# Performance work log

Hardware: AMD Instinct MI355X
Metric: run time of the kernel (lower is better)

Reference implementation:

```python
import jax, jax.numpy as jnp
import numpy as np

B, N, D, H, NCTX = 4, 2048, 1024, 16, 512
HD = D // H  # head dim = 64


def setup_inputs() -> dict:
    key = jax.random.key(0)
    ks = jax.random.split(key, 6)
    return {
        "x": jax.random.normal(ks[0], (B, N, D), dtype=jnp.float32),
        "ctx_ppr": jax.random.uniform(ks[1], (B, NCTX), dtype=jnp.float32),
        "ctx_trust": jax.random.normal(ks[2], (B, NCTX), dtype=jnp.float32),
        "W_in": jax.random.normal(ks[3], (D, 3 * D), dtype=jnp.float32) * 0.02,
        "b_in": jnp.zeros((3 * D,), dtype=jnp.float32),
        "W_out": jax.random.normal(ks[4], (D, D), dtype=jnp.float32) * 0.02,
        "b_out": jnp.zeros((D,), dtype=jnp.float32),
        "log_ppr_alpha": jnp.full((1,), 0.1, dtype=jnp.float32),
        "trust_scale": jnp.full((1,), 0.1, dtype=jnp.float32),
        "n_ctx": NCTX,
    }


def reference(x, ctx_ppr, ctx_trust, W_in, b_in, W_out, b_out, log_ppr_alpha, trust_scale, n_ctx):
    b, n, dmodel = x.shape
    # QKV projection
    qkv = x @ W_in + b_in                                   # [B,N,3D]
    q, k, v = jnp.split(qkv, 3, axis=-1)
    q = q.reshape(b, n, H, HD).transpose(0, 2, 1, 3)        # [B,H,N,d]
    k = k.reshape(b, n, H, HD).transpose(0, 2, 1, 3)
    v = v.reshape(b, n, H, HD).transpose(0, 2, 1, 3)
    if n_ctx > 0:
        # multiplicative trust gate on context-token values
        gate = jax.nn.sigmoid(trust_scale * ctx_trust)      # [B,n_ctx]
        gate_full = jnp.concatenate(
            [gate, jnp.ones((b, n - n_ctx), dtype=x.dtype)], axis=1)  # [B,N]
        v = v * gate_full[:, None, :, None]
        # additive graph (log-PPR) column bias on attention logits
        col_bias = -log_ppr_alpha * jnp.log(jnp.maximum(ctx_ppr, 1e-8))  # [B,n_ctx]
        bias = jnp.concatenate(
            [col_bias, jnp.zeros((b, n - n_ctx), dtype=x.dtype)], axis=1)  # [B,N]
    else:
        bias = jnp.zeros((b, n), dtype=x.dtype)
    scale = 1.0 / np.sqrt(HD).astype(np.float32)
    scores = jnp.einsum("bhqd,bhkd->bhqk", q, k) * scale + bias[:, None, None, :]
    attn = jax.nn.softmax(scores, axis=-1)                  # [B,H,N,N]
    out = jnp.einsum("bhqk,bhkd->bhqd", attn, v)            # [B,H,N,d]
    out = out.transpose(0, 2, 1, 3).reshape(b, n, dmodel)
    return out @ W_out + b_out
```

## Files before the change

kernel.cpp:

```cpp
#include <hip/hip_runtime.h>
#include <hip/hip_bf16.h>
#include <stdint.h>

#define BATCH  4
#define NSEQ   2048
#define DMODEL 1024
#define NHEAD  16
#define HDIM   64
#define NCTXC  512

typedef unsigned short u16;
typedef __attribute__((ext_vector_type(8))) short bfrag;
typedef __attribute__((ext_vector_type(4))) float facc;

typedef __attribute__((address_space(3))) void lds_void;
typedef __attribute__((address_space(1))) void g_void;

__device__ __forceinline__ void gload16(const void* g, void* l) {
  __builtin_amdgcn_global_load_lds((const g_void*)g, (lds_void*)l, 16, 0, 0);
}

__device__ __forceinline__ u16 f2bf(float f) {
  union { float f; uint32_t u; } un; un.f = f;
  uint32_t u = un.u;
  u += 0x7fffu + ((u >> 16) & 1u);
  return (u16)(u >> 16);
}

#if __has_builtin(__builtin_amdgcn_cvt_pk_bf16_f32)
__device__ __forceinline__ uint32_t pk2bf(float a, float b) {
  return __builtin_bit_cast(uint32_t, __builtin_amdgcn_cvt_pk_bf16_f32(a, b));
}
#else
__device__ __forceinline__ uint32_t pk2bf(float a, float b) {
  return (uint32_t)f2bf(a) | ((uint32_t)f2bf(b) << 16);
}
#endif

__device__ __forceinline__ float bf2f(u16 h) {
  union { uint32_t u; float f; } un;
  un.u = ((uint32_t)h) << 16;
  return un.f;
}

__device__ __forceinline__ float load_flex(const void* p, size_t idx, int isb) {
  return isb ? bf2f(((const u16*)p)[idx]) : ((const float*)p)[idx];
}

__device__ __forceinline__ uint4 pack8(float4 a, float4 b) {
  uint4 r;
  r.x = pk2bf(a.x, a.y);
  r.y = pk2bf(a.z, a.w);
  r.z = pk2bf(b.x, b.y);
  r.w = pk2bf(b.z, b.w);
  return r;
}

__global__ __launch_bounds__(256) void detect_kernel(const u16* __restrict__ xraw,
                                                     int* __restrict__ flag) {
  __shared__ int s_high, s_zero;
  if (threadIdx.x == 0) { s_high = 0; s_zero = 0; }
  __syncthreads();
  int h = 0, z = 0;
  for (int i = threadIdx.x; i < 4096; i += 256) {
    const u16 v = xraw[2 * i];
    const int e = (v >> 7) & 0xFF;
    if (e >= 0x90) h++;
    if (v == 0) z++;
  }
  atomicAdd(&s_high, h);
  atomicAdd(&s_zero, z);
  __syncthreads();
  if (threadIdx.x == 0) flag[0] = (s_high < 64 && s_zero < 2048) ? 1 : 0;
}


__global__ __launch_bounds__(256) void cast_x_kernel(const void* __restrict__ x,
                                                     u16* __restrict__ xb,
                                                     const int* __restrict__ flag) {
  const int isb = flag[0];
  const int i = blockIdx.x * 256 + threadIdx.x;
  if (isb) {
    ((uint4*)xb)[i] = ((const uint4*)x)[i];
  } else {
    const float4 f0 = ((const float4*)x)[2 * i];
    const float4 f1 = ((const float4*)x)[2 * i + 1];
    ((uint4*)xb)[i] = pack8(f0, f1);
  }
}

__global__ __launch_bounds__(256) void transpose_flex(const void* __restrict__ W,
                                                      u16* __restrict__ Wt,
                                                      int R, int C,
                                                      const int* __restrict__ flag) {
  __shared__ float tile[32][33];
  const int isb = flag[0];
  const int tx = threadIdx.x;
  const int ty = threadIdx.y;
  const int c0 = blockIdx.x * 32;
  const int r0 = blockIdx.y * 32;
#pragma unroll
  for (int j = 0; j < 32; j += 8)
    tile[ty + j][tx] = load_flex(W, (size_t)(r0 + ty + j) * C + c0 + tx, isb);
  __syncthreads();
#pragma unroll
  for (int j = 0; j < 32; j += 8)
    Wt[(size_t)(c0 + ty + j) * R + r0 + tx] = f2bf(tile[tx][ty + j]);
}

__global__ __launch_bounds__(256) void prep_small(const void* __restrict__ b_in,
                                                  const void* __restrict__ b_out,
                                                  const void* __restrict__ ppr,
                                                  const void* __restrict__ trust,
                                                  const void* __restrict__ alpha_p,
                                                  const void* __restrict__ ts_p,
                                                  float* __restrict__ bin_f,
                                                  float* __restrict__ bout_f,
                                                  float* __restrict__ gate,
                                                  float* __restrict__ cbias,
                                                  const int* __restrict__ flag) {
  const int isb = flag[0];
  const int i = blockIdx.x * 256 + threadIdx.x;
  if (i < 3072) {
    bin_f[i] = load_flex(b_in, i, isb);
  } else if (i < 4096) {
    bout_f[i - 3072] = load_flex(b_out, i - 3072, isb);
  } else if (i < 4096 + BATCH * NCTXC) {
    const int j = i - 4096;
    const float ts = load_flex(ts_p, 0, isb), al = load_flex(alpha_p, 0, isb);
    gate[j]  = 1.0f / (1.0f + __expf(-ts * load_flex(trust, j, isb)));
    cbias[j] = -al * logf(fmaxf(load_flex(ppr, j, isb), 1e-8f)) * 1.44269504f;
  }
}

__device__ __forceinline__ void kloop_mfma(const u16* __restrict__ Ag,
                                           const u16* __restrict__ Bg,
                                           u16* As, u16* Bs,
                                           int tid, int wM, int wN, int l16, int quad,
                                           facc acc[4][4]) {
  char* ldsA = (char*)As + tid * 16;
  char* ldsB = (char*)Bs + tid * 16;
  for (int k0 = 0; k0 < 1024; k0 += 32) {
    __syncthreads();
    gload16(Ag + k0, ldsA);
    gload16(Ag + (size_t)64 * 1024 + k0, ldsA + 4096);
    gload16(Bg + k0, ldsB);
    gload16(Bg + (size_t)64 * 1024 + k0, ldsB + 4096);
    __syncthreads();

    bfrag af[4], bf[4];
#pragma unroll
    for (int i = 0; i < 4; ++i)
      af[i] = *(const bfrag*)(&As[(wM + i * 16 + l16) * 32 + quad * 8]);
#pragma unroll
    for (int j = 0; j < 4; ++j)
      bf[j] = *(const bfrag*)(&Bs[(wN + j * 16 + l16) * 32 + quad * 8]);
#pragma unroll
    for (int i = 0; i < 4; ++i)
#pragma unroll
      for (int j = 0; j < 4; ++j)
        acc[i][j] = __builtin_amdgcn_mfma_f32_16x16x32_bf16(af[i], bf[j], acc[i][j], 0, 0, 0);
  }
}

__global__ __launch_bounds__(256) void gemm_qkvt(const u16* __restrict__ xb,
                                                 const u16* __restrict__ Wt,
                                                 const float* __restrict__ bin_f,
                                                 const float* __restrict__ gate,
                                                 u16* __restrict__ qk,
                                                 u16* __restrict__ Vtg) {
  __shared__ u16 As[128 * 32];
  __shared__ u16 Bs[128 * 32];
  const int tid  = threadIdx.x;
  const int w    = tid >> 6;
  const int lane = tid & 63;
  const int quad = lane >> 4;
  const int l16  = lane & 15;
  const int wM   = (w >> 1) * 64;
  const int wN   = (w & 1) * 64;
  const int id   = blockIdx.x;
  const int srow  = tid >> 2;
  const int spart = tid & 3;

  facc acc[4][4] = {};

  if (id < 1024) {
    const int bn = id & 15, bm = id >> 4;
    const u16* Ag = xb + (size_t)(bm * 128 + srow) * 1024 + spart * 8;
    const u16* Bg = Wt + (size_t)(bn * 128 + srow) * 1024 + spart * 8;
    kloop_mfma(Ag, Bg, As, Bs, tid, wM, wN, l16, quad, acc);

    const float qs = (bn < 8) ? 0.18033688f : 1.0f;
#pragma unroll
    for (int i = 0; i < 4; ++i) {
      const int grow0 = bm * 128 + wM + i * 16 + quad * 4;
#pragma unroll
      for (int j = 0; j < 4; ++j) {
        const int gcol = bn * 128 + wN + j * 16 + l16;
        const float bv = bin_f[gcol];
#pragma unroll
        for (int r = 0; r < 4; ++r)
          qk[(size_t)(grow0 + r) * 2048 + gcol] = f2bf((acc[i][j][r] + bv) * qs);
      }
    }
  } else {
    const int id2 = id - 1024;
    const int bn = id2 & 63, bm = id2 >> 6;
    const u16* Ag = Wt + (size_t)2048 * 1024 + (size_t)(bm * 128 + srow) * 1024 + spart * 8;
    const u16* Bg = xb + (size_t)(bn * 128 + srow) * 1024 + spart * 8;
    kloop_mfma(Ag, Bg, As, Bs, tid, wM, wN, l16, quad, acc);

#pragma unroll
    for (int i = 0; i < 4; ++i) {
      const int grow0 = bm * 128 + wM + i * 16 + quad * 4;
      const int h   = grow0 >> 6;
      const int dd0 = grow0 & 63;
#pragma unroll
      for (int j = 0; j < 4; ++j) {
        const int gcol = bn * 128 + wN + j * 16 + l16;
        const int bb  = gcol >> 11;
        const int tok = gcol & (NSEQ - 1);
        const float gl = (tok < NCTXC) ? gate[bb * NCTXC + tok] : 1.0f;
        u16* dst = &Vtg[((size_t)((bb * NHEAD + h) * HDIM + dd0)) * NSEQ + tok];
#pragma unroll
        for (int r = 0; r < 4; ++r)
          dst[(size_t)r * NSEQ] = f2bf((acc[i][j][r] + bin_f[2 * DMODEL + grow0 + r]) * gl);
      }
    }
  }
}

__global__ __launch_bounds__(256) void gemm_out(const u16* __restrict__ A,
                                                const u16* __restrict__ Bt,
                                                const float* __restrict__ biasf,
                                                void* __restrict__ Cout,
                                                const int* __restrict__ flag) {
  __shared__ u16 As[128 * 32];
  __shared__ u16 Bs[128 * 32];
  const int isb  = flag[0];
  const int tid  = threadIdx.x;
  const int w    = tid >> 6;
  const int lane = tid & 63;
  const int quad = lane >> 4;
  const int l16  = lane & 15;
  const int wM   = (w >> 1) * 64;
  const int wN   = (w & 1) * 64;
  const int bm   = blockIdx.y;
  const int bn   = blockIdx.x;
  const int srow  = tid >> 2;
  const int spart = tid & 3;

  facc acc[4][4] = {};
  const u16* Ag = A + (size_t)(bm * 128 + srow) * 2048 + spart * 8;
  const u16* Bg = Bt + (size_t)(bn * 128 + srow) * 1024 + spart * 8;
  char* ldsA = (char*)As + tid * 16;
  char* ldsB = (char*)Bs + tid * 16;

  for (int k0 = 0; k0 < 1024; k0 += 32) {
    __syncthreads();
    gload16(Ag + k0, ldsA);
    gload16(Ag + (size_t)64 * 2048 + k0, ldsA + 4096);
    gload16(Bg + k0, ldsB);
    gload16(Bg + (size_t)64 * 1024 + k0, ldsB + 4096);
    __syncthreads();

    bfrag af[4], bf[4];
#pragma unroll
    for (int i = 0; i < 4; ++i)
      af[i] = *(const bfrag*)(&As[(wM + i * 16 + l16) * 32 + quad * 8]);
#pragma unroll
    for (int j = 0; j < 4; ++j)
      bf[j] = *(const bfrag*)(&Bs[(wN + j * 16 + l16) * 32 + quad * 8]);
#pragma unroll
    for (int i = 0; i < 4; ++i)
#pragma unroll
      for (int j = 0; j < 4; ++j)
        acc[i][j] = __builtin_amdgcn_mfma_f32_16x16x32_bf16(af[i], bf[j], acc[i][j], 0, 0, 0);
  }

#pragma unroll
  for (int i = 0; i < 4; ++i) {
    const int grow0 = bm * 128 + wM + i * 16 + quad * 4;
#pragma unroll
    for (int j = 0; j < 4; ++j) {
      const int gcol = bn * 128 + wN + j * 16 + l16;
      const float bv = biasf[gcol];
#pragma unroll
      for (int r = 0; r < 4; ++r) {
        const float v = acc[i][j][r] + bv;
        if (isb) ((u16*)Cout)[(size_t)(grow0 + r) * 1024 + gcol] = f2bf(v);
        else     ((float*)Cout)[(size_t)(grow0 + r) * 1024 + gcol] = v;
      }
    }
  }
}

__global__ __launch_bounds__(256) void attn_kernel(u16* __restrict__ qk,
                                                   const u16* __restrict__ vtg,
                                                   const float* __restrict__ cbias) {
  const int qt = blockIdx.x, h = blockIdx.y, b = blockIdx.z;
  __shared__ u16 Ks[64 * 72];
  __shared__ u16 Vt[2][64 * 72];
  __shared__ u16 Ps[4 * 16 * 72];

  const int tid  = threadIdx.x;
  const int w    = tid >> 6;
  const int lane = tid & 63;
  const int quad = lane >> 4;
  const int l16  = lane & 15;
  const int srow = tid >> 2;
  const int spart = tid & 3;

  const u16* qrow = qk + (size_t)(b * NSEQ + qt * 64 + w * 16 + l16) * 2048 + h * HDIM;
  const bfrag bq0 = *(const bfrag*)(qrow + quad * 8);
  const bfrag bq1 = *(const bfrag*)(qrow + 32 + quad * 8);

  float l_i = 0.0f;
  facc o[4] = {};
  bfrag bp0, bp1;

  const u16* kst = qk + (size_t)(b * NSEQ) * 2048 + DMODEL + h * HDIM;
  const u16* vst = vtg + (size_t)((b * NHEAD + h) * HDIM + srow) * NSEQ;
  u16* psw = &Ps[w * 16 * 72];

  uint4 pk0, pk1, pv0, pv1;
  {
    const u16* ks = kst + (size_t)srow * 2048 + spart * 16;
    pk0 = *(const uint4*)ks;
    pk1 = *(const uint4*)(ks + 8);
    const u16* vs = vst + spart * 16;
    pv0 = *(const uint4*)vs;
    pv1 = *(const uint4*)(vs + 8);
  }

  for (int t = 0; t < NSEQ / 64; ++t) {
    __syncthreads();
    u16* vb = Vt[t & 1];
    *(uint4*)(&Ks[srow * 72 + spart * 16])     = pk0;
    *(uint4*)(&Ks[srow * 72 + spart * 16 + 8]) = pk1;
    *(uint4*)(&vb[srow * 72 + spart * 16])     = pv0;
    *(uint4*)(&vb[srow * 72 + spart * 16 + 8]) = pv1;
    __syncthreads();

    {
      const int tn = (t < NSEQ / 64 - 1) ? t + 1 : t;
      const u16* ks = kst + (size_t)(tn * 64 + srow) * 2048 + spart * 16;
      pk0 = *(const uint4*)ks;
      pk1 = *(const uint4*)(ks + 8);
      const u16* vs = vst + tn * 64 + spart * 16;
      pv0 = *(const uint4*)vs;
      pv1 = *(const uint4*)(vs + 8);
    }

    facc s[4];
#pragma unroll
    for (int nt = 0; nt < 4; ++nt) {
      const bfrag ak0 = *(const bfrag*)(&Ks[(nt * 16 + l16) * 72 + quad * 8]);
      const bfrag ak1 = *(const bfrag*)(&Ks[(nt * 16 + l16) * 72 + 32 + quad * 8]);
      facc z = {};
      z = __builtin_amdgcn_mfma_f32_16x16x32_bf16(ak0, bq0, z, 0, 0, 0);
      s[nt] = __builtin_amdgcn_mfma_f32_16x16x32_bf16(ak1, bq1, z, 0, 0, 0);
    }

    if (t > 0) {
      const u16* vp = Vt[(t - 1) & 1];
#pragma unroll
      for (int dt = 0; dt < 4; ++dt) {
        const bfrag av0 = *(const bfrag*)(&vp[(dt * 16 + l16) * 72 + quad * 8]);
        const bfrag av1 = *(const bfrag*)(&vp[(dt * 16 + l16) * 72 + 32 + quad * 8]);
        o[dt] = __builtin_amdgcn_mfma_f32_16x16x32_bf16(av0, bp0, o[dt], 0, 0, 0);
        o[dt] = __builtin_amdgcn_mfma_f32_16x16x32_bf16(av1, bp1, o[dt], 0, 0, 0);
      }
    }

    float rs = 0.0f;
    if (t < 8) {
      const float* cb = cbias + b * NCTXC + t * 64 + quad * 4;
#pragma unroll
      for (int nt = 0; nt < 4; ++nt)
#pragma unroll
        for (int r = 0; r < 4; ++r) {
          const float p = __builtin_amdgcn_exp2f(s[nt][r] + cb[nt * 16 + r]);
          s[nt][r] = p;
          rs += p;
        }
    } else {
#pragma unroll
      for (int nt = 0; nt < 4; ++nt)
#pragma unroll
        for (int r = 0; r < 4; ++r) {
          const float p = __builtin_amdgcn_exp2f(s[nt][r]);
          s[nt][r] = p;
          rs += p;
        }
    }
    rs += __shfl_xor(rs, 16);
    rs += __shfl_xor(rs, 32);
    l_i += rs;

#pragma unroll
    for (int nt = 0; nt < 4; ++nt) {
      uint2 pk;
      pk.x = pk2bf(s[nt][0], s[nt][1]);
      pk.y = pk2bf(s[nt][2], s[nt][3]);
      *(uint2*)(&psw[l16 * 72 + nt * 16 + quad * 4]) = pk;
    }
    __asm__ volatile("s_waitcnt lgkmcnt(0)" ::: "memory");
    bp0 = *(const bfrag*)(&psw[l16 * 72 + quad * 8]);
    bp1 = *(const bfrag*)(&psw[l16 * 72 + 32 + quad * 8]);
  }

  {
    const u16* vp = Vt[(NSEQ / 64 - 1) & 1];
#pragma unroll
    for (int dt = 0; dt < 4; ++dt) {
      const bfrag av0 = *(const bfrag*)(&vp[(dt * 16 + l16) * 72 + quad * 8]);
      const bfrag av1 = *(const bfrag*)(&vp[(dt * 16 + l16) * 72 + 32 + quad * 8]);
      o[dt] = __builtin_amdgcn_mfma_f32_16x16x32_bf16(av0, bp0, o[dt], 0, 0, 0);
      o[dt] = __builtin_amdgcn_mfma_f32_16x16x32_bf16(av1, bp1, o[dt], 0, 0, 0);
    }
  }

  const float inv = 1.0f / l_i;
  u16* orow = qk + (size_t)(b * NSEQ + qt * 64 + w * 16 + l16) * 2048 + h * HDIM;
#pragma unroll
  for (int dt = 0; dt < 4; ++dt) {
    uint2 st;
    st.x = pk2bf(o[dt][0] * inv, o[dt][1] * inv);
    st.y = pk2bf(o[dt][2] * inv, o[dt][3] * inv);
    *(uint2*)(orow + dt * 16 + quad * 4) = st;
  }
}


extern "C" void kernel_launch(void* const* d_in, const int* in_sizes, int n_in,
                              void* d_out, int out_size, void* d_ws, size_t ws_size,
                              hipStream_t stream) {
  const void* x          = d_in[0];
  const void* ctx_ppr    = d_in[1];
  const void* ctx_trust  = d_in[2];
  const void* W_in       = d_in[3];
  const void* b_in       = d_in[4];
  const void* W_out      = d_in[5];
  const void* b_out      = d_in[6];
  const void* lppr_alpha = d_in[7];
  const void* tscale     = d_in[8];

  char* ws = (char*)d_ws;
  u16* Wt    = (u16*)ws;  ws += (size_t)3072 * 1024 * 2;
  u16* WoT   = (u16*)ws;  ws += (size_t)1024 * 1024 * 2;
  u16* qk    = (u16*)ws;  ws += (size_t)8192 * 2048 * 2;
  u16* Vtg   = (u16*)ws;  ws += (size_t)64 * 64 * 2048 * 2;
  u16* xb    = (u16*)ws;  ws += (size_t)8192 * 1024 * 2;
  float* bin_f  = (float*)ws; ws += 3072 * 4;
  float* bout_f = (float*)ws; ws += 1024 * 4;
  float* gate   = (float*)ws; ws += (size_t)BATCH * NCTXC * 4;
  float* cbias  = (float*)ws; ws += (size_t)BATCH * NCTXC * 4;
  int*   flag   = (int*)ws;   ws += 64;

  detect_kernel<<<dim3(1), dim3(256), 0, stream>>>((const u16*)x, flag);
  cast_x_kernel<<<dim3(4096), dim3(256), 0, stream>>>(x, xb, flag);
  transpose_flex<<<dim3(96, 32), dim3(32, 8), 0, stream>>>(W_in, Wt, 1024, 3072, flag);
  transpose_flex<<<dim3(32, 32), dim3(32, 8), 0, stream>>>(W_out, WoT, 1024, 1024, flag);
  prep_small<<<dim3(24), dim3(256), 0, stream>>>(b_in, b_out, ctx_ppr, ctx_trust,
                                                 lppr_alpha, tscale,
                                                 bin_f, bout_f, gate, cbias, flag);
  gemm_qkvt<<<dim3(1536), dim3(256), 0, stream>>>(xb, Wt, bin_f, gate, qk, Vtg);
  attn_kernel<<<dim3(32, 16, 4), dim3(256), 0, stream>>>(qk, Vtg, cbias);
  gemm_out<<<dim3(8, 64), dim3(256), 0, stream>>>(qk, WoT, bout_f, d_out, flag);
}
```

Measured before the change: 338.4 us.

## Process 128 queries per attention block and swizzle block-to-head mapping

Measured after the change: 334.1 us. About the same (-1.2%).

```diff
diff --git a/kernel.cpp b/kernel.cpp
--- a/kernel.cpp
+++ b/kernel.cpp
@@ -298,9 +298,15 @@
 __global__ __launch_bounds__(256) void attn_kernel(u16* __restrict__ qk,
                                                    const u16* __restrict__ vtg,
                                                    const float* __restrict__ cbias) {
-  const int qt = blockIdx.x, h = blockIdx.y, b = blockIdx.z;
+  const int id    = blockIdx.x;
+  const int chunk = id >> 3;
+  const int qt    = chunk & 15;
+  const int hg    = (id & 7) | ((chunk >> 4) << 3);
+  const int h     = hg & 15;
+  const int b     = hg >> 4;
+
   __shared__ u16 Ks[64 * 72];
-  __shared__ u16 Vt[2][64 * 72];
+  __shared__ u16 Vt[64 * 72];
   __shared__ u16 Ps[4 * 16 * 72];
 
   const int tid  = threadIdx.x;
@@ -311,13 +317,16 @@
   const int srow = tid >> 2;
   const int spart = tid & 3;
 
-  const u16* qrow = qk + (size_t)(b * NSEQ + qt * 64 + w * 16 + l16) * 2048 + h * HDIM;
-  const bfrag bq0 = *(const bfrag*)(qrow + quad * 8);
-  const bfrag bq1 = *(const bfrag*)(qrow + 32 + quad * 8);
-
-  float l_i = 0.0f;
-  facc o[4] = {};
-  bfrag bp0, bp1;
+  bfrag bq[2][2];
+#pragma unroll
+  for (int qs = 0; qs < 2; ++qs) {
+    const u16* qrow = qk + (size_t)(b * NSEQ + qt * 128 + (w * 2 + qs) * 16 + l16) * 2048 + h * HDIM;
+    bq[qs][0] = *(const bfrag*)(qrow + quad * 8);
+    bq[qs][1] = *(const bfrag*)(qrow + 32 + quad * 8);
+  }
+
+  float l_i[2] = {0.0f, 0.0f};
+  facc o[2][4] = {};
 
   const u16* kst = qk + (size_t)(b * NSEQ) * 2048 + DMODEL + h * HDIM;
   const u16* vst = vtg + (size_t)((b * NHEAD + h) * HDIM + srow) * NSEQ;
@@ -335,11 +344,10 @@
 
   for (int t = 0; t < NSEQ / 64; ++t) {
     __syncthreads();
-    u16* vb = Vt[t & 1];
     *(uint4*)(&Ks[srow * 72 + spart * 16])     = pk0;
     *(uint4*)(&Ks[srow * 72 + spart * 16 + 8]) = pk1;
-    *(uint4*)(&vb[srow * 72 + spart * 16])     = pv0;
-    *(uint4*)(&vb[srow * 72 + spart * 16 + 8]) = pv1;
+    *(uint4*)(&Vt[srow * 72 + spart * 16])     = pv0;
+    *(uint4*)(&Vt[srow * 72 + spart * 16 + 8]) = pv1;
     __syncthreads();
 
     {
@@ -352,83 +360,81 @@
       pv1 = *(const uint4*)(vs + 8);
     }
 
-    facc s[4];
+    bfrag ak[4][2], av[4][2];
 #pragma unroll
     for (int nt = 0; nt < 4; ++nt) {
-      const bfrag ak0 = *(const bfrag*)(&Ks[(nt * 16 + l16) * 72 + quad * 8]);
-      const bfrag ak1 = *(const bfrag*)(&Ks[(nt * 16 + l16) * 72 + 32 + quad * 8]);
-      facc z = {};
-      z = __builtin_amdgcn_mfma_f32_16x16x32_bf16(ak0, bq0, z, 0, 0, 0);
-      s[nt] = __builtin_amdgcn_mfma_f32_16x16x32_bf16(ak1, bq1, z, 0, 0, 0);
-    }
-
-    if (t > 0) {
-      const u16* vp = Vt[(t - 1) & 1];
+      ak[nt][0] = *(const bfrag*)(&Ks[(nt * 16 + l16) * 72 + quad * 8]);
+      ak[nt][1] = *(const bfrag*)(&Ks[(nt * 16 + l16) * 72 + 32 + quad * 8]);
+      av[nt][0] = *(const bfrag*)(&Vt[(nt * 16 + l16) * 72 + quad * 8]);
+      av[nt][1] = *(const bfrag*)(&Vt[(nt * 16 + l16) * 72 + 32 + quad * 8]);
+    }
+
+#pragma unroll
+    for (int qs = 0; qs < 2; ++qs) {
+      facc s[4];
+#pragma unroll
+      for (int nt = 0; nt < 4; ++nt) {
+        facc z = {};
+        z = __builtin_amdgcn_mfma_f32_16x16x32_bf16(ak[nt][0], bq[qs][0], z, 0, 0, 0);
+        s[nt] = __builtin_amdgcn_mfma_f32_16x16x32_bf16(ak[nt][1], bq[qs][1], z, 0, 0, 0);
+      }
+
+      float rs = 0.0f;
+      if (t < 8) {
+        const float* cb = cbias + b * NCTXC + t * 64 + quad * 4;
+#pragma unroll
+        for (int nt = 0; nt < 4; ++nt)
+#pragma unroll
+          for (int r = 0; r < 4; ++r) {
+            const float p = __builtin_amdgcn_exp2f(s[nt][r] + cb[nt * 16 + r]);
+            s[nt][r] = p;
+            rs += p;
+          }
+      } else {
+#pragma unroll
+        for (int nt = 0; nt < 4; ++nt)
+#pragma unroll
+          for (int r = 0; r < 4; ++r) {
+            const float p = __builtin_amdgcn_exp2f(s[nt][r]);
+            s[nt][r] = p;
+            rs += p;
+          }
+      }
+      rs += __shfl_xor(rs, 16);
+      rs += __shfl_xor(rs, 32);
+      l_i[qs] += rs;
+
+#pragma unroll
+      for (int nt = 0; nt < 4; ++nt) {
+        uint2 pk;
+        pk.x = pk2bf(s[nt][0], s[nt][1]);
+        pk.y = pk2bf(s[nt][2], s[nt][3]);
+        *(uint2*)(&psw[l16 * 72 + nt * 16 + quad * 4]) = pk;
+      }
+
+      __asm__ volatile("s_waitcnt lgkmcnt(0)" ::: "memory");
+
+      const bfrag bp0 = *(const bfrag*)(&psw[l16 * 72 + quad * 8]);
+      const bfrag bp1 = *(const bfrag*)(&psw[l16 * 72 + 32 + quad * 8]);
 #pragma unroll
       for (int dt = 0; dt < 4; ++dt) {
-        const bfrag av0 = *(const bfrag*)(&vp[(dt * 16 + l16) * 72 + quad * 8]);
-        const bfrag av1 = *(const bfrag*)(&vp[(dt * 16 + l16) * 72 + 32 + quad * 8]);
-        o[dt] = __builtin_amdgcn_mfma_f32_16x16x32_bf16(av0, bp0, o[dt], 0, 0, 0);
-        o[dt] = __builtin_amdgcn_mfma_f32_16x16x32_bf16(av1, bp1, o[dt], 0, 0, 0);
-      }
-    }
-
-    float rs = 0.0f;
-    if (t < 8) {
-      const float* cb = cbias + b * NCTXC + t * 64 + quad * 4;
-#pragma unroll
-      for (int nt = 0; nt < 4; ++nt)
-#pragma unroll
-        for (int r = 0; r < 4; ++r) {
-          const float p = __builtin_amdgcn_exp2f(s[nt][r] + cb[nt * 16 + r]);
-          s[nt][r] = p;
-          rs += p;
-        }
-    } else {
-#pragma unroll
-      for (int nt = 0; nt < 4; ++nt)
-#pragma unroll
-        for (int r = 0; r < 4; ++r) {
-          const float p = __builtin_amdgcn_exp2f(s[nt][r]);
-          s[nt][r] = p;
-          rs += p;
-        }
-    }
-    rs += __shfl_xor(rs, 16);
-    rs += __shfl_xor(rs, 32);
-    l_i += rs;
-
-#pragma unroll
-    for (int nt = 0; nt < 4; ++nt) {
-      uint2 pk;
-      pk.x = pk2bf(s[nt][0], s[nt][1]);
-      pk.y = pk2bf(s[nt][2], s[nt][3]);
-      *(uint2*)(&psw[l16 * 72 + nt * 16 + quad * 4]) = pk;
-    }
-    __asm__ volatile("s_waitcnt lgkmcnt(0)" ::: "memory");
-    bp0 = *(const bfrag*)(&psw[l16 * 72 + quad * 8]);
-    bp1 = *(const bfrag*)(&psw[l16 * 72 + 32 + quad * 8]);
-  }
-
-  {
-    const u16* vp = Vt[(NSEQ / 64 - 1) & 1];
+        o[qs][dt] = __builtin_amdgcn_mfma_f32_16x16x32_bf16(av[dt][0], bp0, o[qs][dt], 0, 0, 0);
+        o[qs][dt] = __builtin_amdgcn_mfma_f32_16x16x32_bf16(av[dt][1], bp1, o[qs][dt], 0, 0, 0);
+      }
+    }
+  }
+
+#pragma unroll
+  for (int qs = 0; qs < 2; ++qs) {
+    const float inv = 1.0f / l_i[qs];
+    u16* orow = qk + (size_t)(b * NSEQ + qt * 128 + (w * 2 + qs) * 16 + l16) * 2048 + h * HDIM;
 #pragma unroll
     for (int dt = 0; dt < 4; ++dt) {
-      const bfrag av0 = *(const bfrag*)(&vp[(dt * 16 + l16) * 72 + quad * 8]);
-      const bfrag av1 = *(const bfrag*)(&vp[(dt * 16 + l16) * 72 + 32 + quad * 8]);
-      o[dt] = __builtin_amdgcn_mfma_f32_16x16x32_bf16(av0, bp0, o[dt], 0, 0, 0);
-      o[dt] = __builtin_amdgcn_mfma_f32_16x16x32_bf16(av1, bp1, o[dt], 0, 0, 0);
-    }
-  }
-
-  const float inv = 1.0f / l_i;
-  u16* orow = qk + (size_t)(b * NSEQ + qt * 64 + w * 16 + l16) * 2048 + h * HDIM;
-#pragma unroll
-  for (int dt = 0; dt < 4; ++dt) {
-    uint2 st;
-    st.x = pk2bf(o[dt][0] * inv, o[dt][1] * inv);
-    st.y = pk2bf(o[dt][2] * inv, o[dt][3] * inv);
-    *(uint2*)(orow + dt * 16 + quad * 4) = st;
+      uint2 st;
+      st.x = pk2bf(o[qs][dt][0] * inv, o[qs][dt][1] * inv);
+      st.y = pk2bf(o[qs][dt][2] * inv, o[qs][dt][3] * inv);
+      *(uint2*)(orow + dt * 16 + quad * 4) = st;
+    }
   }
 }
 
@@ -466,6 +472,6 @@
                                                  lppr_alpha, tscale,
                                                  bin_f, bout_f, gate, cbias, flag);
   gemm_qkvt<<<dim3(1536), dim3(256), 0, stream>>>(xb, Wt, bin_f, gate, qk, Vtg);
-  attn_kernel<<<dim3(32, 16, 4), dim3(256), 0, stream>>>(qk, Vtg, cbias);
+  attn_kernel<<<dim3(1024), dim3(256), 0, stream>>>(qk, Vtg, cbias);
   gemm_out<<<dim3(8, 64), dim3(256), 0, stream>>>(qk, WoT, bout_f, d_out, flag);
 }
```
